# Optimization experiments

Measured on AMD Instinct MI355X. Metric: run time of the kernel, lower is better.

## Reference

```python
import jax, jax.numpy as jnp
import numpy as np

EPS = 1e-8

def setup_inputs() -> dict:
    key = jax.random.key(0)
    kq, kk, kc, ks = jax.random.split(key, 4)
    d, m, K, Q, N = 128, 128, 4, 512, 131072
    query = jax.random.normal(kq, (Q, d), jnp.float32)
    keys = jax.random.normal(kk, (N, d), jnp.float32)
    # per-coordinate MSE codebook centers (sorted), scaled for unit-norm vectors in R^d
    codebook = jnp.sort(jax.random.normal(kc, (K,), jnp.float32)) / jnp.sqrt(jnp.float32(d))
    # QJL random projection matrix S: (m, d)
    S = jax.random.normal(ks, (m, d), jnp.float32)
    return {"query": query, "keys": keys, "codebook": codebook, "S": S}

def reference(query, keys, codebook, S):
    m = S.shape[0]
    # --- quantize(keys): Algorithm 2 ---
    vec_norm = jnp.linalg.norm(keys, axis=-1)                    # (N,)  ||x||
    x_norm = keys / (vec_norm[:, None] + EPS)                    # normalize
    # Stage 1: MSE codebook quantize (per-coordinate nearest center)
    idx = jnp.argmin(jnp.abs(x_norm[..., None] - codebook), axis=-1)  # (N, d)
    x_mse = codebook[idx]                                        # dequantize (gather)
    # residual
    r = x_norm - x_mse                                           # (N, d)
    r_norm = jnp.linalg.norm(r, axis=-1)                         # (N,)
    # Stage 2: QJL sign quantization of projected residual
    signs = jnp.where(r @ S.T >= 0, 1.0, -1.0).astype(keys.dtype)  # (N, m)
    # --- inner_product(query, compressed) ---
    term1 = query @ x_mse.T                                      # (Q, N)  <q, k_mse>
    Sq = query @ S.T                                             # (Q, m)
    scale = jnp.sqrt(jnp.pi / 2.0) / m
    term2 = (Sq @ signs.T) * (r_norm * scale)[None, :]           # QJL correction
    return (term1 + term2) * vec_norm[None, :]                   # rescale by ||k||
```

## Files before the change

### kernel.cpp

```cpp
#include <hip/hip_runtime.h>
#include <stdint.h>


typedef __attribute__((ext_vector_type(8))) short bf16x8;
typedef __attribute__((ext_vector_type(4))) float f32x4;

__device__ __forceinline__ uint16_t f2bf(float x) {
    uint32_t u = __builtin_bit_cast(uint32_t, x);
    uint32_t r = (u + 0x7fffu + ((u >> 16) & 1u)) >> 16;
    return (uint16_t)r;
}

__device__ __forceinline__ void load_lds16(const void* g, void* l) {
    __builtin_amdgcn_global_load_lds(
        (const __attribute__((address_space(1))) void*)g,
        (__attribute__((address_space(3))) void*)l, 16, 0, 0);
}

__global__ __launch_bounds__(256) void prep_keys(
    const float* __restrict__ keys, const float* __restrict__ codebook,
    uint16_t* __restrict__ Bhat, float* __restrict__ rout,
    float* __restrict__ wout, int N)
{
    __shared__ float r_rm[16 * 132];
    __shared__ float rtmp[128];
    __shared__ float vn_sh[16];

    const int tid = threadIdx.x;
    const float c0 = codebook[0], c1 = codebook[1], c2 = codebook[2], c3 = codebook[3];
    const float scale = 0.009791516697777346f;

    for (int tile = 0; tile < 16; ++tile) {
        const int n0 = blockIdx.x * 256 + tile * 16;
        __syncthreads();

        #pragma unroll
        for (int u = 0; u < 2; ++u) {
            int f = u * 256 + tid;
            int row = f >> 5;
            int i0 = (f & 31) * 4;
            float4 v = ((const float4*)(keys + (size_t)(n0 + row) * 128))[f & 31];
            *(float4*)&r_rm[row * 132 + i0] = v;
        }
        __syncthreads();

        if (tid < 128) {
            int row = tid >> 3, k = tid & 7;
            const float* x = &r_rm[row * 132];
            float a;
            {
                #pragma clang fp contract(off)
                float x0 = x[k];
                a = x0 * x0;
                for (int t = 1; t < 16; ++t) {
                    float xv = x[t * 8 + k];
                    a = a + xv * xv;
                }
            }
            rtmp[tid] = a;
        }
        __syncthreads();

        if (tid < 16) {
            const float* r = &rtmp[tid * 8];
            float res = ((r[0] + r[1]) + (r[2] + r[3])) + ((r[4] + r[5]) + (r[6] + r[7]));
            vn_sh[tid] = sqrtf(res);
        }
        __syncthreads();

        {
            int row = tid >> 4, i0 = (tid & 15) * 8;
            float vn = vn_sh[row];
            float denom = vn + 1e-8f;
            float rsq = 0.f;
            uint32_t pk[4];
            float rloc[8];
            #pragma unroll
            for (int u = 0; u < 8; ++u) {
                float xv = r_rm[row * 132 + i0 + u];
                float xn = xv / denom;
                float b = c0, d = fabsf(xn - c0), t;
                t = fabsf(xn - c1); if (t < d) { d = t; b = c1; }
                t = fabsf(xn - c2); if (t < d) { d = t; b = c2; }
                t = fabsf(xn - c3); if (t < d) { d = t; b = c3; }
                float rv = xn - b;
                rloc[u] = rv;
                rsq += rv * rv;
                uint32_t bv = f2bf(vn * b);
                if (u & 1) pk[u >> 1] |= bv << 16; else pk[u >> 1] = bv;
            }
            *(uint4*)(Bhat + (size_t)(n0 + row) * 256 + i0) = *(uint4*)pk;
            float* rp = rout + (size_t)(n0 + row) * 128 + i0;
            *(float4*)rp       = *(float4*)&rloc[0];
            *(float4*)(rp + 4) = *(float4*)&rloc[4];
            #pragma unroll
            for (int off2 = 1; off2 < 16; off2 <<= 1) rsq += __shfl_xor(rsq, off2);
            if ((tid & 15) == 0) wout[n0 + row] = sqrtf(rsq) * scale * vn;
        }
    }
}

__global__ __launch_bounds__(256) void sign_dots(
    const float* __restrict__ r, const float* __restrict__ w,
    const float* __restrict__ S, uint16_t* __restrict__ Bhat, int N)
{
    __shared__ float S_lds[128 * 132];
    const int tid = threadIdx.x;
    const int lane = tid & 63;
    const int wid = tid >> 6;

    for (int f = tid; f < 4096; f += 256) {
        float4 v = ((const float4*)S)[f];
        int j = f >> 5, i0 = (f & 31) * 4;
        *(float4*)&S_lds[j * 132 + i0] = v;
    }
    __syncthreads();

    const int j = ((wid & 1) << 6) | lane;
    const float* Sj = &S_lds[j * 132];
    const int rowsel = (wid >> 1) * 8;

    for (int tile = 0; tile < 16; ++tile) {
        const int n0 = blockIdx.x * 256 + tile * 16 + rowsel;
        const float* rb = r + (size_t)n0 * 128;
        float acc[8] = {0.f, 0.f, 0.f, 0.f, 0.f, 0.f, 0.f, 0.f};
        #pragma unroll 4
        for (int i0 = 0; i0 < 128; i0 += 4) {
            float4 sv = *(const float4*)(Sj + i0);
            #pragma unroll
            for (int k = 0; k < 8; ++k) {
                float4 rv = *(const float4*)(rb + k * 128 + i0);
                acc[k] = __builtin_fmaf(rv.x, sv.x, acc[k]);
                acc[k] = __builtin_fmaf(rv.y, sv.y, acc[k]);
                acc[k] = __builtin_fmaf(rv.z, sv.z, acc[k]);
                acc[k] = __builtin_fmaf(rv.w, sv.w, acc[k]);
            }
        }
        #pragma unroll
        for (int k = 0; k < 8; ++k) {
            float wv = w[n0 + k];
            float v = (acc[k] >= 0.f) ? wv : -wv;
            Bhat[(size_t)(n0 + k) * 256 + 128 + j] = f2bf(v);
        }
    }
}

__global__ __launch_bounds__(256) void prep_A(
    const float* __restrict__ query, const float* __restrict__ S,
    uint16_t* __restrict__ Ahat)
{
    int gid = blockIdx.x * 256 + threadIdx.x;
    int q = gid >> 7, j = gid & 127;
    const float4* qr = (const float4*)(query + (size_t)q * 128);
    const float4* sr = (const float4*)(S + (size_t)j * 128);
    float acc = 0.f;
    #pragma unroll
    for (int i = 0; i < 32; ++i) {
        float4 a = qr[i], b = sr[i];
        acc += a.x * b.x + a.y * b.y + a.z * b.z + a.w * b.w;
    }
    Ahat[(size_t)q * 256 + j] = f2bf(query[(size_t)q * 128 + j]);
    Ahat[(size_t)q * 256 + 128 + j] = f2bf(acc);
}

__global__ __launch_bounds__(256) void gemm_bt(
    const uint16_t* __restrict__ A, const uint16_t* __restrict__ B,
    float* __restrict__ C, int N, int Q)
{
    __shared__ uint16_t Asl[128 * 64];
    __shared__ uint16_t Bsl[128 * 64];
    const int tid = threadIdx.x;
    const int lane = tid & 63, wid = tid >> 6;

    const int nbn = N >> 7, nbm = Q >> 7;
    const int f = blockIdx.x;
    int bm_idx, bn_idx;
    if ((nbn & 7) == 0) {
        const int xcd = f & 7, s = f >> 3;
        const int pxb = nbn >> 3;
        const int sq = s / nbm;
        bn_idx = xcd * pxb + sq;
        bm_idx = s - sq * nbm;
    } else {
        bn_idx = f % nbn;
        bm_idx = f / nbn;
    }
    const int bm = bm_idx * 128;
    const int bn = bn_idx * 128;

    const int wm = (wid & 1) * 64, wn = (wid >> 1) * 64;
    const int lrow = lane & 15, lquad = lane >> 4;
    f32x4 acc[4][4] = {};

    #pragma unroll
    for (int kc = 0; kc < 256; kc += 64) {
        __syncthreads();
        #pragma unroll
        for (int u = 0; u < 4; ++u) {
            int flat = u * 256 + tid;
            int row = flat >> 3, ch = flat & 7;
            load_lds16(A + (size_t)(bm + row) * 256 + kc + ch * 8, &Asl[flat * 8]);
            load_lds16(B + (size_t)(bn + row) * 256 + kc + ch * 8, &Bsl[flat * 8]);
        }
        __syncthreads();
        #pragma unroll
        for (int ks = 0; ks < 2; ++ks) {
            bf16x8 af[4], bfr[4];
            #pragma unroll
            for (int ff = 0; ff < 4; ++ff) {
                af[ff]  = *(const bf16x8*)&Asl[(wm + ff * 16 + lrow) * 64 + ks * 32 + lquad * 8];
                bfr[ff] = *(const bf16x8*)&Bsl[(wn + ff * 16 + lrow) * 64 + ks * 32 + lquad * 8];
            }
            #pragma unroll
            for (int i = 0; i < 4; ++i)
                #pragma unroll
                for (int jj = 0; jj < 4; ++jj)
                    acc[i][jj] = __builtin_amdgcn_mfma_f32_16x16x32_bf16(af[i], bfr[jj], acc[i][jj], 0, 0, 0);
        }
    }

    #pragma unroll
    for (int i = 0; i < 4; ++i) {
        int row = bm + wm + i * 16 + lquad * 4;
        #pragma unroll
        for (int jj = 0; jj < 4; ++jj) {
            int col = bn + wn + jj * 16 + lrow;
            float* cp = C + (size_t)row * N + col;
            #pragma unroll
            for (int rr = 0; rr < 4; ++rr) cp[(size_t)rr * N] = acc[i][jj][rr];
        }
    }
}

extern "C" void kernel_launch(void* const* d_in, const int* in_sizes, int n_in,
                              void* d_out, int out_size, void* d_ws, size_t ws_size,
                              hipStream_t stream) {
    const float* query    = (const float*)d_in[0];
    const float* keys     = (const float*)d_in[1];
    const float* codebook = (const float*)d_in[2];
    const float* S        = (const float*)d_in[3];
    const int Q = in_sizes[0] / 128;
    const int N = in_sizes[1] / 128;

    uint16_t* Bhat = (uint16_t*)d_ws;
    uint16_t* Ahat = (uint16_t*)((char*)d_ws + (size_t)N * 256 * 2);

    float* r_ws = (float*)d_out;
    float* w_ws = (float*)d_out + (size_t)N * 128;

    prep_keys<<<N / 256, 256, 0, stream>>>(keys, codebook, Bhat, r_ws, w_ws, N);
    sign_dots<<<N / 256, 256, 0, stream>>>(r_ws, w_ws, S, Bhat, N);
    prep_A<<<(Q * 128) / 256, 256, 0, stream>>>(query, S, Ahat);
    gemm_bt<<<(N / 128) * (Q / 128), 256, 0, stream>>>(Ahat, Bhat, (float*)d_out, N, Q);
}
```

Before: 624.5 us.

## Hold S rows in registers and read residuals via scalar constant loads in sign_dots

sign_dots no longer stages S into LDS. Each thread keeps its full 128-float S row in registers, and the residual rows and weights are read through address-space-4 (constant) pointers with a wave-uniform row offset, so the compiler can emit scalar loads shared by the whole wave. The grid grows fourfold and each block handles 64 keys instead of 256, which spreads the work across more CUs. The trade-off is heavy VGPR use for the 128-float S row plus the accumulators, which may lower occupancy. It also relies on constant-address-space loads of data that the previous kernel just wrote.

```diff
diff --git a/kernel.cpp b/kernel.cpp
--- a/kernel.cpp
+++ b/kernel.cpp
@@ -4,6 +4,9 @@
 
 typedef __attribute__((ext_vector_type(8))) short bf16x8;
 typedef __attribute__((ext_vector_type(4))) float f32x4;
+
+typedef const __attribute__((address_space(4))) float  cf1;
+typedef const __attribute__((address_space(4))) f32x4  cf4;
 
 __device__ __forceinline__ uint16_t f2bf(float x) {
     uint32_t u = __builtin_bit_cast(uint32_t, x);
@@ -104,41 +107,36 @@
     const float* __restrict__ r, const float* __restrict__ w,
     const float* __restrict__ S, uint16_t* __restrict__ Bhat, int N)
 {
-    __shared__ float S_lds[128 * 132];
     const int tid = threadIdx.x;
     const int lane = tid & 63;
     const int wid = tid >> 6;
-
-    for (int f = tid; f < 4096; f += 256) {
-        float4 v = ((const float4*)S)[f];
-        int j = f >> 5, i0 = (f & 31) * 4;
-        *(float4*)&S_lds[j * 132 + i0] = v;
-    }
-    __syncthreads();
-
     const int j = ((wid & 1) << 6) | lane;
-    const float* Sj = &S_lds[j * 132];
-    const int rowsel = (wid >> 1) * 8;
-
-    for (int tile = 0; tile < 16; ++tile) {
-        const int n0 = blockIdx.x * 256 + tile * 16 + rowsel;
-        const float* rb = r + (size_t)n0 * 128;
+    const int rowsel = __builtin_amdgcn_readfirstlane((wid >> 1) * 8);
+
+    f32x4 Sv[32];
+    const f32x4* Srow = (const f32x4*)(S + (size_t)j * 128);
+    #pragma unroll
+    for (int c = 0; c < 32; ++c) Sv[c] = Srow[c];
+
+    for (int tile = 0; tile < 4; ++tile) {
+        const int n0 = blockIdx.x * 64 + tile * 16 + rowsel;
+        cf4* rb4 = (cf4*)(uintptr_t)(r + (size_t)n0 * 128);
         float acc[8] = {0.f, 0.f, 0.f, 0.f, 0.f, 0.f, 0.f, 0.f};
-        #pragma unroll 4
-        for (int i0 = 0; i0 < 128; i0 += 4) {
-            float4 sv = *(const float4*)(Sj + i0);
+        #pragma unroll
+        for (int c = 0; c < 32; ++c) {
+            f32x4 sv = Sv[c];
             #pragma unroll
             for (int k = 0; k < 8; ++k) {
-                float4 rv = *(const float4*)(rb + k * 128 + i0);
-                acc[k] = __builtin_fmaf(rv.x, sv.x, acc[k]);
-                acc[k] = __builtin_fmaf(rv.y, sv.y, acc[k]);
-                acc[k] = __builtin_fmaf(rv.z, sv.z, acc[k]);
-                acc[k] = __builtin_fmaf(rv.w, sv.w, acc[k]);
+                f32x4 rv = rb4[k * 32 + c];
+                acc[k] = __builtin_fmaf(rv[0], sv[0], acc[k]);
+                acc[k] = __builtin_fmaf(rv[1], sv[1], acc[k]);
+                acc[k] = __builtin_fmaf(rv[2], sv[2], acc[k]);
+                acc[k] = __builtin_fmaf(rv[3], sv[3], acc[k]);
             }
         }
         #pragma unroll
         for (int k = 0; k < 8; ++k) {
-            float wv = w[n0 + k];
+            float wv = *(cf1*)(uintptr_t)(w + n0 + k);
             float v = (acc[k] >= 0.f) ? wv : -wv;
             Bhat[(size_t)(n0 + k) * 256 + 128 + j] = f2bf(v);
         }
@@ -249,7 +247,7 @@
     float* w_ws = (float*)d_out + (size_t)N * 128;
 
     prep_keys<<<N / 256, 256, 0, stream>>>(keys, codebook, Bhat, r_ws, w_ws, N);
-    sign_dots<<<N / 256, 256, 0, stream>>>(r_ws, w_ws, S, Bhat, N);
+    sign_dots<<<N / 64, 256, 0, stream>>>(r_ws, w_ws, S, Bhat, N);
     prep_A<<<(Q * 128) / 256, 256, 0, stream>>>(query, S, Ahat);
     gemm_bt<<<(N / 128) * (Q / 128), 256, 0, stream>>>(Ahat, Bhat, (float*)d_out, N, Q);
 }
```

Result: slower. 874.1 us (+40.0%).
